# Performance work log

Measured on AMD Instinct MI355X. Metric: run time of the kernel, lower is better.

The kernel has to match this reference:

```python
import jax, jax.numpy as jnp
import numpy as np

INPUT_DIM = 256
UNITS = 256
BATCH = 65536


def _glorot(key, shape):
    fan_in, fan_out = shape
    limit = np.sqrt(6.0 / (fan_in + fan_out)).astype(np.float32)
    return jax.random.uniform(key, shape, jnp.float32, -limit, limit)


def setup_inputs() -> dict:
    key = jax.random.key(0)
    ks = jax.random.split(key, 8)
    d = {
        "inputs": jax.random.normal(ks[0], (BATCH, INPUT_DIM), jnp.float32),
        "h_prev": jax.random.normal(ks[1], (BATCH, UNITS), jnp.float32),
        "c_prev": jax.random.normal(ks[2], (BATCH, UNITS), jnp.float32),
        "W_f": _glorot(ks[3], (INPUT_DIM + UNITS, UNITS)),
        "W_i": _glorot(ks[4], (INPUT_DIM + UNITS, UNITS)),
        "W_c": _glorot(ks[5], (INPUT_DIM + UNITS, UNITS)),
        "W_o": _glorot(ks[6], (INPUT_DIM + UNITS, UNITS)),
        "b_f": jnp.zeros((UNITS,), jnp.float32),
        "b_i": jnp.zeros((UNITS,), jnp.float32),
        "b_c": jnp.zeros((UNITS,), jnp.float32),
        "b_o": jnp.zeros((UNITS,), jnp.float32),
    }
    return d


def reference(inputs, h_prev, c_prev, W_f, W_i, W_c, W_o, b_f, b_i, b_c, b_o):
    # z: [B, input_dim + units]
    z = jnp.concatenate([inputs, h_prev], axis=-1)
    f = jax.nn.sigmoid(z @ W_f + b_f)
    i = jax.nn.sigmoid(z @ W_i + b_i)
    c_tilde = jnp.tanh(z @ W_c + b_c)
    c = f * c_prev + i * c_tilde
    o = jax.nn.sigmoid(z @ W_o + b_o)
    h = o * jnp.tanh(c)
    return h, c
```

## Files before the change

### kernel.cpp

```cpp
#include <hip/hip_runtime.h>
#include <hip/hip_bf16.h>
#include <stdint.h>

#define BATCH   65536
#define UNITS   256
#define NCHUNK  8
#define ROWP    68
#define GSZ     (64 * ROWP)
#define SMEM_BYTES 34816

using f32x16 = __attribute__((ext_vector_type(16))) float;
using bf16x8 = __attribute__((ext_vector_type(8))) short;

__device__ __forceinline__ short f2bf(float f) {
  union { float f; unsigned u; } v; v.f = f;
  unsigned r = v.u + 0x7FFFu + ((v.u >> 16) & 1u);
  return (short)(r >> 16);
}
__device__ __forceinline__ float bf2f(short s) {
  union { float f; unsigned u; } v; v.u = ((unsigned)(unsigned short)s) << 16;
  return v.f;
}
__device__ __forceinline__ unsigned pk2(float a, float b) {
  union { __hip_bfloat162 h; unsigned u; } cv;
  cv.h = __float22bfloat162_rn(make_float2(a, b));
  return cv.u;
}
__device__ __forceinline__ bf16x8 cvt8(float4 a, float4 b) {
  union { unsigned u[4]; bf16x8 v; } r;
  r.u[0] = pk2(a.x, a.y); r.u[1] = pk2(a.z, a.w);
  r.u[2] = pk2(b.x, b.y); r.u[3] = pk2(b.z, b.w);
  return r.v;
}

#define BAR() do { asm volatile("s_waitcnt lgkmcnt(0)" ::: "memory"); \
                   __builtin_amdgcn_s_barrier(); } while (0)

__global__ void cvt_weights(const float* __restrict__ Wf, const float* __restrict__ Wi,
                            const float* __restrict__ Wc, const float* __restrict__ Wo,
                            short* __restrict__ Wt) {
  int idx = blockIdx.x * 256 + threadIdx.x;
  int g   = idx >> 17;
  int k   = (idx >> 8) & 511;
  int col = idx & 255;
  const float* W = (g == 0) ? Wf : (g == 1) ? Wi : (g == 2) ? Wc : Wo;
  float val = W[k * 256 + col];
  int nb = col >> 6, n = col & 63;
  int c = k >> 6, kg = (k >> 3) & 7, k8 = k & 7;
  int out = ((((g * 4 + nb) * 8 + c) * 8 + kg) * 64 + n) * 8 + k8;
  Wt[out] = f2bf(val);
}

__global__ __launch_bounds__(256, 3) void lstm_fused(
    const float* __restrict__ x, const float* __restrict__ hprev,
    const float* __restrict__ cprev, const short* __restrict__ Wt,
    const float* __restrict__ bfp, const float* __restrict__ bip,
    const float* __restrict__ bcp, const float* __restrict__ bop,
    float* __restrict__ hout, float* __restrict__ cout)
{
  extern __shared__ __align__(16) char smem[];
  const int tid  = threadIdx.x;
  const int g    = tid >> 6;
  const int lane = tid & 63;
  const int la   = lane & 31;
  const int hh   = lane >> 5;

  int bid = blockIdx.x;
  int wg  = (bid & 7) * 512 + (bid >> 3);
  const int m0 = (wg >> 2) * 64;
  const int nb = wg & 3;
  const int n0 = nb * 64;

  const short* Bbase = Wt + ((size_t)(g * 4 + nb)) * 32768 + hh * 512 + la * 8;

  f32x16 acc[2][2] = {};
  bf16x8 breg[8];
  float4 vA[2][4];

  const int arow  = tid >> 2;
  const int q     = tid & 3;
  const int slotW = (arow ^ (q << 2)) & 63;

  auto ldA = [&](int c, float4* v) {
    const float* base = (c < 4) ? x : hprev;
    const float* rowp = base + (size_t)(m0 + arow) * 256 + (c & 3) * 64;
    v[0] = *(const float4*)(rowp + q * 8);
    v[1] = *(const float4*)(rowp + q * 8 + 4);
    v[2] = *(const float4*)(rowp + (q + 4) * 8);
    v[3] = *(const float4*)(rowp + (q + 4) * 8 + 4);
  };
  auto wrA = [&](int buf, const float4* v) {
    char* Ab = smem + buf * 8192;
    *(bf16x8*)(Ab + q * 1024 + slotW * 16)       = cvt8(v[0], v[1]);
    *(bf16x8*)(Ab + (q + 4) * 1024 + slotW * 16) = cvt8(v[2], v[3]);
  };
  auto loadB = [&](int c, int ks) {
    const short* Bc = Bbase + (size_t)c * 4096 + ks * 1024;
    breg[2 * ks]     = *(const bf16x8*)(Bc);
    breg[2 * ks + 1] = *(const bf16x8*)(Bc + 256);
  };

  const int ccol = tid & 63;
  const int rg   = tid >> 6;
  const size_t gbase = (size_t)(m0 + rg * 16) * 256 + n0 + ccol;

  ldA(0, vA[0]);
  ldA(1, vA[1]);
  wrA(0, vA[0]);
#pragma unroll
  for (int ks = 0; ks < 4; ++ks) loadB(0, ks);
  ldA(2, vA[0]);
  float cp[16];
#pragma unroll
  for (int j = 0; j < 16; ++j) cp[j] = cprev[gbase + (size_t)j * 256];
  BAR();

  int buf = 0;
#pragma unroll
  for (int c = 0; c < NCHUNK; ++c) {
    if (c + 1 < NCHUNK) wrA(buf ^ 1, vA[(c + 1) & 1]);
    if (c + 3 < NCHUNK) ldA(c + 3, vA[(c + 3) & 1]);
    const char*  Ab = smem + buf * 8192;
    const short* Bn = Bbase + (size_t)((c + 1) & 7) * 4096;
#pragma unroll
    for (int ks = 0; ks < 4; ++ks) {
      const int kg   = 2 * ks + hh;
      const int slot = la ^ ((kg & 3) << 2);
      const int off  = kg * 1024 + slot * 16;
      bf16x8 a0 = *(const bf16x8*)(Ab + off);
      bf16x8 a1 = *(const bf16x8*)(Ab + off + 512);
      acc[0][0] = __builtin_amdgcn_mfma_f32_32x32x16_bf16(a0, breg[2*ks],   acc[0][0], 0, 0, 0);
      acc[0][1] = __builtin_amdgcn_mfma_f32_32x32x16_bf16(a0, breg[2*ks+1], acc[0][1], 0, 0, 0);
      acc[1][0] = __builtin_amdgcn_mfma_f32_32x32x16_bf16(a1, breg[2*ks],   acc[1][0], 0, 0, 0);
      acc[1][1] = __builtin_amdgcn_mfma_f32_32x32x16_bf16(a1, breg[2*ks+1], acc[1][1], 0, 0, 0);
      breg[2*ks]     = *(const bf16x8*)(Bn + ks * 1024);
      breg[2*ks + 1] = *(const bf16x8*)(Bn + ks * 1024 + 256);
    }
    BAR();
    buf ^= 1;
  }

  const float* bptr = (g == 0) ? bfp : (g == 1) ? bip : (g == 2) ? bcp : bop;
  const float bias0 = bptr[n0 + la];
  const float bias1 = bptr[n0 + 32 + la];
  short* G = (short*)smem;
#pragma unroll
  for (int mi = 0; mi < 2; ++mi)
#pragma unroll
    for (int ni = 0; ni < 2; ++ni) {
      const float bias = ni ? bias1 : bias0;
      const int   col  = la + ni * 32;
#pragma unroll
      for (int rq = 0; rq < 4; ++rq) {
        const int row0 = rq * 8 + 4 * hh + mi * 32;
        float t[4];
#pragma unroll
        for (int e = 0; e < 4; ++e) {
          float vv = acc[mi][ni][rq * 4 + e] + bias;
          t[e] = (g == 2) ? (1.f - 2.f / (__expf(2.f * vv) + 1.f))
                          : (1.f / (1.f + __expf(-vv)));
        }
        uint2 u; u.x = pk2(t[0], t[1]); u.y = pk2(t[2], t[3]);
        *(uint2*)(G + g * GSZ + col * ROWP + row0) = u;
      }
    }
  BAR();

  {
    const short* Gp = G + ccol * ROWP + rg * 16;
    bf16x8 gf[4][2];
#pragma unroll
    for (int gg = 0; gg < 4; ++gg) {
      gf[gg][0] = *(const bf16x8*)(Gp + gg * GSZ);
      gf[gg][1] = *(const bf16x8*)(Gp + gg * GSZ + 8);
    }
#pragma unroll
    for (int j = 0; j < 16; ++j) {
      float fg = bf2f(gf[0][j >> 3][j & 7]);
      float ig = bf2f(gf[1][j >> 3][j & 7]);
      float cg = bf2f(gf[2][j >> 3][j & 7]);
      float og = bf2f(gf[3][j >> 3][j & 7]);
      float cnew = fg * cp[j] + ig * cg;
      float hnew = og * (1.f - 2.f / (__expf(2.f * cnew) + 1.f));
      hout[gbase + (size_t)j * 256] = hnew;
      cout[gbase + (size_t)j * 256] = cnew;
    }
  }
}

extern "C" void kernel_launch(void* const* d_in, const int* in_sizes, int n_in,
                              void* d_out, int out_size, void* d_ws, size_t ws_size,
                              hipStream_t stream) {
  const float* x     = (const float*)d_in[0];
  const float* hprev = (const float*)d_in[1];
  const float* cprev = (const float*)d_in[2];
  const float* Wf    = (const float*)d_in[3];
  const float* Wi    = (const float*)d_in[4];
  const float* Wc    = (const float*)d_in[5];
  const float* Wo    = (const float*)d_in[6];
  const float* bfp   = (const float*)d_in[7];
  const float* bip   = (const float*)d_in[8];
  const float* bcp   = (const float*)d_in[9];
  const float* bop   = (const float*)d_in[10];
  float* out = (float*)d_out;
  short* Wt  = (short*)d_ws;

  cvt_weights<<<2048, 256, 0, stream>>>(Wf, Wi, Wc, Wo, Wt);

  lstm_fused<<<dim3(4096), dim3(256), SMEM_BYTES, stream>>>(
      x, hprev, cprev, Wt, bfp, bip, bcp, bop,
      out, out + (size_t)BATCH * UNITS);
}
```

Measured before the change: 167.8 us.

## Restructure LSTM GEMM pipeline to cut registers and raise occupancy to four

Raises launch bounds from 3 to 4 waves-per-SIMD blocks. To fit, it drops the two-deep prefetch of A-tile float4 registers down to a single buffer, replaces the rolling per-k-step B register reload with two whole-chunk B register sets (ping-pong), and defers the c_prev loads until after the GEMM loop. The aim is to hide memory latency through more resident waves instead of deep software prefetching. The cost is a shallower prefetch distance for A and c_prev loads that are no longer overlapped with the matrix work.

```diff
diff --git a/kernel.cpp b/kernel.cpp
--- a/kernel.cpp
+++ b/kernel.cpp
@@ -51,7 +51,7 @@
   Wt[out] = f2bf(val);
 }
 
-__global__ __launch_bounds__(256, 3) void lstm_fused(
+__global__ __launch_bounds__(256, 4) void lstm_fused(
     const float* __restrict__ x, const float* __restrict__ hprev,
     const float* __restrict__ cprev, const short* __restrict__ Wt,
     const float* __restrict__ bfp, const float* __restrict__ bip,
@@ -74,14 +74,14 @@
   const short* Bbase = Wt + ((size_t)(g * 4 + nb)) * 32768 + hh * 512 + la * 8;
 
   f32x16 acc[2][2] = {};
-  bf16x8 breg[8];
-  float4 vA[2][4];
+  bf16x8 bregA[8], bregB[8];
+  float4 v[4];
 
   const int arow  = tid >> 2;
   const int q     = tid & 3;
   const int slotW = (arow ^ (q << 2)) & 63;
 
-  auto ldA = [&](int c, float4* v) {
+  auto ldA = [&](int c) {
     const float* base = (c < 4) ? x : hprev;
     const float* rowp = base + (size_t)(m0 + arow) * 256 + (c & 3) * 64;
     v[0] = *(const float4*)(rowp + q * 8);
@@ -89,39 +89,21 @@
     v[2] = *(const float4*)(rowp + (q + 4) * 8);
     v[3] = *(const float4*)(rowp + (q + 4) * 8 + 4);
   };
-  auto wrA = [&](int buf, const float4* v) {
+  auto wrA = [&](int buf) {
     char* Ab = smem + buf * 8192;
     *(bf16x8*)(Ab + q * 1024 + slotW * 16)       = cvt8(v[0], v[1]);
     *(bf16x8*)(Ab + (q + 4) * 1024 + slotW * 16) = cvt8(v[2], v[3]);
   };
-  auto loadB = [&](int c, int ks) {
-    const short* Bc = Bbase + (size_t)c * 4096 + ks * 1024;
-    breg[2 * ks]     = *(const bf16x8*)(Bc);
-    breg[2 * ks + 1] = *(const bf16x8*)(Bc + 256);
-  };
-
-  const int ccol = tid & 63;
-  const int rg   = tid >> 6;
-  const size_t gbase = (size_t)(m0 + rg * 16) * 256 + n0 + ccol;
-
-  ldA(0, vA[0]);
-  ldA(1, vA[1]);
-  wrA(0, vA[0]);
-#pragma unroll
-  for (int ks = 0; ks < 4; ++ks) loadB(0, ks);
-  ldA(2, vA[0]);
-  float cp[16];
-#pragma unroll
-  for (int j = 0; j < 16; ++j) cp[j] = cprev[gbase + (size_t)j * 256];
-  BAR();
-
-  int buf = 0;
-#pragma unroll
-  for (int c = 0; c < NCHUNK; ++c) {
-    if (c + 1 < NCHUNK) wrA(buf ^ 1, vA[(c + 1) & 1]);
-    if (c + 3 < NCHUNK) ldA(c + 3, vA[(c + 3) & 1]);
-    const char*  Ab = smem + buf * 8192;
-    const short* Bn = Bbase + (size_t)((c + 1) & 7) * 4096;
+  auto loadB = [&](int c, bf16x8* br) {
+#pragma unroll
+    for (int ks = 0; ks < 4; ++ks) {
+      const short* Bc = Bbase + (size_t)c * 4096 + ks * 1024;
+      br[2 * ks]     = *(const bf16x8*)(Bc);
+      br[2 * ks + 1] = *(const bf16x8*)(Bc + 256);
+    }
+  };
+  auto compute = [&](int buf, const bf16x8* br) {
+    const char* Ab = smem + buf * 8192;
 #pragma unroll
     for (int ks = 0; ks < 4; ++ks) {
       const int kg   = 2 * ks + hh;
@@ -129,16 +111,41 @@
       const int off  = kg * 1024 + slot * 16;
       bf16x8 a0 = *(const bf16x8*)(Ab + off);
       bf16x8 a1 = *(const bf16x8*)(Ab + off + 512);
-      acc[0][0] = __builtin_amdgcn_mfma_f32_32x32x16_bf16(a0, breg[2*ks],   acc[0][0], 0, 0, 0);
-      acc[0][1] = __builtin_amdgcn_mfma_f32_32x32x16_bf16(a0, breg[2*ks+1], acc[0][1], 0, 0, 0);
-      acc[1][0] = __builtin_amdgcn_mfma_f32_32x32x16_bf16(a1, breg[2*ks],   acc[1][0], 0, 0, 0);
-      acc[1][1] = __builtin_amdgcn_mfma_f32_32x32x16_bf16(a1, breg[2*ks+1], acc[1][1], 0, 0, 0);
-      breg[2*ks]     = *(const bf16x8*)(Bn + ks * 1024);
-      breg[2*ks + 1] = *(const bf16x8*)(Bn + ks * 1024 + 256);
-    }
+      acc[0][0] = __builtin_amdgcn_mfma_f32_32x32x16_bf16(a0, br[2*ks],   acc[0][0], 0, 0, 0);
+      acc[0][1] = __builtin_amdgcn_mfma_f32_32x32x16_bf16(a0, br[2*ks+1], acc[0][1], 0, 0, 0);
+      acc[1][0] = __builtin_amdgcn_mfma_f32_32x32x16_bf16(a1, br[2*ks],   acc[1][0], 0, 0, 0);
+      acc[1][1] = __builtin_amdgcn_mfma_f32_32x32x16_bf16(a1, br[2*ks+1], acc[1][1], 0, 0, 0);
+    }
+  };
+
+  ldA(0);
+  wrA(0);
+  loadB(0, bregA);
+  ldA(1);
+  BAR();
+
+#pragma unroll
+  for (int cc = 0; cc < NCHUNK; cc += 2) {
+    wrA(1);
+    loadB(cc + 1, bregB);
+    if (cc + 2 < NCHUNK) ldA(cc + 2);
+    compute(0, bregA);
     BAR();
-    buf ^= 1;
+    if (cc + 2 < NCHUNK) {
+      wrA(0);
+      loadB(cc + 2, bregA);
+    }
+    if (cc + 3 < NCHUNK) ldA(cc + 3);
+    compute(1, bregB);
+    BAR();
   }
+
+  const int ccol = tid & 63;
+  const int rg   = tid >> 6;
+  const size_t gbase = (size_t)(m0 + rg * 16) * 256 + n0 + ccol;
+  float cp[16];
+#pragma unroll
+  for (int j = 0; j < 16; ++j) cp[j] = cprev[gbase + (size_t)j * 256];
 
   const float* bptr = (g == 0) ? bfp : (g == 1) ? bip : (g == 2) ? bcp : bop;
   const float bias0 = bptr[n0 + la];
```

Result: slower. 347.8 us (+107.2%).
